# Performance work log

Measured on AMD Instinct MI355X. Metric: run time of the kernel, lower is better.

## Reference

```python
import jax, jax.numpy as jnp
import numpy as np
import math

B, S, HID = 1, 2048, 2048
H, QLR, KVLR = 16, 1536, 512
NOPE, ROPE, VD = 128, 64, 128
QKD = NOPE + ROPE


def rmsnorm(x, w, eps=1e-6):
    v = jnp.mean(x * x, axis=-1, keepdims=True)
    return w * (x * jax.lax.rsqrt(v + eps))


def rope_tables(seq_len, dim):
    inv_freq = 1.0 / (10000.0 ** (jnp.arange(0, dim, 2, dtype=jnp.float32) / dim))
    t = jnp.arange(seq_len, dtype=jnp.float32)[:, None]
    freqs = t * inv_freq[None, :]
    freqs = jnp.concatenate([freqs, freqs], axis=-1)  # [S, dim]
    return jnp.cos(freqs), jnp.sin(freqs)


def rotate_half(x):
    x1, x2 = jnp.split(x, 2, axis=-1)
    return jnp.concatenate([-x2, x1], axis=-1)


def setup_inputs() -> dict:
    key = jax.random.key(0)
    ks = jax.random.split(key, 8)
    s = 0.02
    return {
        'x': jax.random.normal(ks[0], (B, S, HID), jnp.float32),
        'wq_a_w': jax.random.normal(ks[1], (QLR, HID), jnp.float32) * s,
        'wq_a_b': jnp.zeros((QLR,), jnp.float32),
        'q_norm_w': jnp.ones((QLR,), jnp.float32),
        'wq_b_w': jax.random.normal(ks[2], (H * QKD, QLR), jnp.float32) * s,
        'wq_b_b': jnp.zeros((H * QKD,), jnp.float32),
        'wkv_a_w': jax.random.normal(ks[3], (KVLR + ROPE, HID), jnp.float32) * s,
        'wkv_a_b': jnp.zeros((KVLR + ROPE,), jnp.float32),
        'kv_norm_w': jnp.ones((KVLR,), jnp.float32),
        'wkv_b_w': jax.random.normal(ks[4], (H * (NOPE + VD), KVLR), jnp.float32) * s,
        'wo_w': jax.random.normal(ks[5], (HID, H * VD), jnp.float32) * s,
        'wo_b': jnp.zeros((HID,), jnp.float32),
    }


def reference(x, wq_a_w, wq_a_b, q_norm_w, wq_b_w, wq_b_b, wkv_a_w, wkv_a_b,
              kv_norm_w, wkv_b_w, wo_w, wo_b):
    bs, seq_len, _ = x.shape
    # low-rank q projection
    q = x @ wq_a_w.T + wq_a_b            # [B,S,QLR]
    q = rmsnorm(q, q_norm_w)
    q = q @ wq_b_w.T + wq_b_b            # [B,S,H*QKD]
    q = q.reshape(bs, seq_len, H, QKD)
    q_nope, q_pe = q[..., :NOPE], q[..., NOPE:]

    # latent kv + rope key
    kv_full = x @ wkv_a_w.T + wkv_a_b    # [B,S,KVLR+ROPE]
    kv, k_pe = kv_full[..., :KVLR], kv_full[..., KVLR:]

    cos, sin = rope_tables(seq_len, ROPE)        # [S,ROPE]
    cos4 = cos[None, :, None, :]
    sin4 = sin[None, :, None, :]
    q_pe = q_pe * cos4 + rotate_half(q_pe) * sin4          # [B,S,H,ROPE]
    k_pe = k_pe * cos[None] + rotate_half(k_pe) * sin[None]  # [B,S,ROPE]

    # absorbed kv projection
    wkv_b = wkv_b_w.reshape(H, NOPE + VD, KVLR)
    q_nope = jnp.einsum('bshd,hdc->bshc', q_nope, wkv_b[:, :NOPE])  # [B,S,H,KVLR]
    kv = rmsnorm(kv, kv_norm_w)                                     # [B,T,KVLR]

    scores = (jnp.einsum('bshc,btc->bsht', q_nope, kv)
              + jnp.einsum('bshr,btr->bsht', q_pe, k_pe)) / math.sqrt(QKD)
    # causal mask: position t > s masked
    s_idx = jnp.arange(seq_len)
    mask = jnp.where(s_idx[None, :, None, None] >= s_idx[None, None, None, :],
                     0.0, -jnp.inf)  # [1,S,1,T]
    scores = jax.nn.softmax(scores + mask, axis=-1)

    out = jnp.einsum('bsht,btc->bshc', scores, kv)            # [B,S,H,KVLR]
    out = jnp.einsum('bshc,hdc->bshd', out, wkv_b[:, NOPE:])  # [B,S,H,VD]
    out = out.reshape(bs, seq_len, H * VD)
    return out @ wo_w.T + wo_b
```

## Files before the change

kernel.cpp:

```cpp
#include <hip/hip_runtime.h>
#include <hip/hip_bf16.h>
#include <stdint.h>


using bf16 = __hip_bfloat16;
typedef __bf16 bf16x8 __attribute__((ext_vector_type(8)));
typedef __bf16 bf16x4 __attribute__((ext_vector_type(4)));
typedef float f32x4 __attribute__((ext_vector_type(4)));

#define S_LEN 2048
#define NHEAD 16

static __device__ __forceinline__ void gload16(const void* g, void* l) {
  __builtin_amdgcn_global_load_lds(
      (const __attribute__((address_space(1))) unsigned int*)g,
      (__attribute__((address_space(3))) unsigned int*)l, 16, 0, 0);
}

__global__ void cvt_all(const float* __restrict__ x, const float* __restrict__ wqa_s,
                        const float* __restrict__ wqb_s, const float* __restrict__ wkva_s,
                        const float* __restrict__ wkvb_s, const float* __restrict__ wo_s,
                        bf16* __restrict__ xb, bf16* __restrict__ wqa,
                        bf16* __restrict__ wqb, bf16* __restrict__ wkva,
                        bf16* __restrict__ wkvb, bf16* __restrict__ wob) {
  const size_t n0 = 1048576;
  const size_t n1 = n0 + 786432;
  const size_t n2 = n1 + 1179648;
  const size_t n3 = n2 + 327680;
  const size_t n4 = n3 + 524288;
  const size_t n5 = n4 + 1048576;
  auto cvt4 = [](const float4 v, bf16* d) {
    bf16x4 o;
    o[0] = (__bf16)__float2bfloat16(v.x);
    o[1] = (__bf16)__float2bfloat16(v.y);
    o[2] = (__bf16)__float2bfloat16(v.z);
    o[3] = (__bf16)__float2bfloat16(v.w);
    *(bf16x4*)d = o;
  };
  for (size_t i = (size_t)blockIdx.x * blockDim.x + threadIdx.x; i < n5;
       i += (size_t)gridDim.x * blockDim.x) {
    if (i < n0) {
      cvt4(*(const float4*)(x + i * 4), xb + i * 4);
    } else if (i < n1) {
      size_t j = i - n0;
      cvt4(*(const float4*)(wqa_s + j * 4), wqa + j * 4);
    } else if (i < n2) {
      size_t j = i - n1;
      cvt4(*(const float4*)(wqb_s + j * 4), wqb + j * 4);
    } else if (i < n3) {
      size_t j = i - n2;
      size_t e = j * 4;
      int r = (int)(e / 2048), c = (int)(e % 2048);
      float4 v = (r < 576) ? *(const float4*)(wkva_s + (size_t)r * 2048 + c)
                           : make_float4(0.f, 0.f, 0.f, 0.f);
      cvt4(v, wkva + e);
    } else if (i < n4) {
      size_t j = i - n3;
      cvt4(*(const float4*)(wkvb_s + j * 4), wkvb + j * 4);
    } else {
      size_t j = i - n4;
      cvt4(*(const float4*)(wo_s + j * 4), wob + j * 4);
    }
  }
}

__global__ void rmsnorm_bf16(const bf16* __restrict__ in, const float* __restrict__ w,
                             bf16* __restrict__ out, int cols) {
  const int r = blockIdx.x, tid = threadIdx.x;
  const bf16* row = in + (size_t)r * cols;
  float ss = 0.f;
  for (int c = tid; c < cols; c += 256) {
    float v = __bfloat162float(row[c]);
    ss += v * v;
  }
  for (int m = 32; m >= 1; m >>= 1) ss += __shfl_xor(ss, m, 64);
  __shared__ float red[4];
  if ((tid & 63) == 0) red[tid >> 6] = ss;
  __syncthreads();
  ss = red[0] + red[1] + red[2] + red[3];
  float inv = rsqrtf(ss / (float)cols + 1e-6f);
  for (int c = tid; c < cols; c += 256)
    out[(size_t)r * cols + c] = __float2bfloat16(__bfloat162float(row[c]) * inv * w[c]);
}

__global__ void kv_post(const float* __restrict__ kvf, const float* __restrict__ kvw,
                        bf16* __restrict__ kvn, bf16* __restrict__ Kh) {
  const int t = blockIdx.x, tid = threadIdx.x;
  const float* row = kvf + (size_t)t * 640;
  float ss = 0.f;
  for (int c = tid; c < 512; c += 256) { float v = row[c]; ss += v * v; }
  for (int m = 32; m >= 1; m >>= 1) ss += __shfl_xor(ss, m, 64);
  __shared__ float red[4];
  if ((tid & 63) == 0) red[tid >> 6] = ss;
  __syncthreads();
  ss = red[0] + red[1] + red[2] + red[3];
  float inv = rsqrtf(ss * (1.0f / 512.0f) + 1e-6f);
  for (int c = tid; c < 512; c += 256)
    kvn[(size_t)t * 512 + c] = __float2bfloat16(row[c] * inv * kvw[c]);
  if (tid < 32) {
    const int j = tid;
    float freq = expf(-(float)j * (1.0f / 32.0f) * 9.210340371976184f);
    float ang = (float)t * freq;
    float cs = cosf(ang), sn = sinf(ang);
    float x1 = row[512 + j];
    float x2 = row[512 + j + 32];
    bf16 o1 = __float2bfloat16(x1 * cs - x2 * sn);
    bf16 o2 = __float2bfloat16(x2 * cs + x1 * sn);
#pragma unroll
    for (int h = 0; h < 16; ++h) {
      bf16* kr = Kh + ((size_t)h * S_LEN + t) * 192 + 128;
      kr[j] = o1;
      kr[j + 32] = o2;
    }
  }
}

__global__ void q_rope(bf16* __restrict__ qv) {
  const int s = blockIdx.x, tid = threadIdx.x;
  for (int it = tid; it < 512; it += 256) {
    const int h = it >> 5, j = it & 31;
    float freq = expf(-(float)j * (1.0f / 32.0f) * 9.210340371976184f);
    float ang = (float)s * freq;
    float cs = cosf(ang), sn = sinf(ang);
    bf16* base = qv + (size_t)s * 3072 + h * 192 + 128;
    float x1 = __bfloat162float(base[j]);
    float x2 = __bfloat162float(base[j + 32]);
    base[j] = __float2bfloat16(x1 * cs - x2 * sn);
    base[j + 32] = __float2bfloat16(x2 * cs + x1 * sn);
  }
}

__global__ __launch_bounds__(256, 2)
void attn_flash(const bf16* __restrict__ qv, const bf16* __restrict__ Kh,
                const bf16* __restrict__ V2T, bf16* __restrict__ oabs) {
  const int lin = (int)blockIdx.x + 32 * (int)blockIdx.y;
  const int l2 = (lin & 7) * 64 + (lin >> 3);
  const int h = l2 >> 5;
  const int qb = 31 - (l2 & 31);
  const int tid = threadIdx.x, w = tid >> 6, lane = tid & 63;
  const int lo = lane & 15, hi = lane >> 4;
  __shared__ bf16 Kn[2][64 * 128];
  __shared__ bf16 Vt[2][128 * 64];
  __shared__ bf16 Pl[4][16 * 72];
  const int q0 = qb * 64 + w * 16;
  const int q = q0 + lo;

  bf16x8 Qf[6];
  {
    const bf16* qp = qv + (size_t)(q0 + lo) * 3072 + h * 192 + hi * 8;
#pragma unroll
    for (int ks = 0; ks < 6; ++ks) Qf[ks] = *(const bf16x8*)(qp + ks * 32);
  }
  f32x4 o[8];
#pragma unroll
  for (int cg = 0; cg < 8; ++cg) o[cg] = (f32x4){0.f, 0.f, 0.f, 0.f};
  float mrow = -3e38f, lrow = 0.f;

  const bf16* khh = Kh + (size_t)h * S_LEN * 192;
  const bf16* vth = V2T + (size_t)h * 128 * S_LEN;

  auto stage = [&](int tt, int b) {
    const int t0s = tt * 64;
#pragma unroll
    for (int i = 0; i < 4; ++i) {
      const int c = w * 4 + i;
      const int row = c * 4 + (lane >> 4);
      gload16(khh + (size_t)(t0s + row) * 192 + (((lane & 15) ^ (row & 7)) << 3),
              &Kn[b][c * 512]);
    }
#pragma unroll
    for (int i = 0; i < 4; ++i) {
      const int c = w * 4 + i;
      const int row = c * 8 + (lane >> 3);
      gload16(vth + (size_t)row * S_LEN + t0s + (((lane & 7) ^ (row & 7)) << 3),
              &Vt[b][c * 512]);
    }
  };

  const int ntile = qb + 1;
  stage(0, 0);
  for (int t = 0; t < ntile; ++t) {
    __syncthreads();
    const int b = t & 1;
    const int t0 = t * 64;

    bf16x8 rk[2][4];
#pragma unroll
    for (int ks2 = 0; ks2 < 2; ++ks2)
#pragma unroll
      for (int f = 0; f < 4; ++f)
        rk[ks2][f] = *(const bf16x8*)(khh + (size_t)(t0 + f * 16 + lo) * 192 + 128 +
                                      ks2 * 32 + hi * 8);

    if (t + 1 < ntile) stage(t + 1, b ^ 1);

    f32x4 sc[4];
#pragma unroll
    for (int f = 0; f < 4; ++f) sc[f] = (f32x4){0.f, 0.f, 0.f, 0.f};
#pragma unroll
    for (int ks = 0; ks < 4; ++ks)
#pragma unroll
      for (int f = 0; f < 4; ++f) {
        const int row = f * 16 + lo;
        bf16x8 kf = *(const bf16x8*)&Kn[b][row * 128 + ((((ks << 2) + hi) ^ (row & 7)) << 3)];
        sc[f] = __builtin_amdgcn_mfma_f32_16x16x32_bf16(kf, Qf[ks], sc[f], 0, 0, 0);
      }
#pragma unroll
    for (int ks2 = 0; ks2 < 2; ++ks2)
#pragma unroll
      for (int f = 0; f < 4; ++f)
        sc[f] = __builtin_amdgcn_mfma_f32_16x16x32_bf16(rk[ks2][f], Qf[4 + ks2], sc[f], 0, 0, 0);

    const bool diag = (t == qb);
    float rmax = -3e38f;
#pragma unroll
    for (int f = 0; f < 4; ++f)
#pragma unroll
      for (int j = 0; j < 4; ++j) {
        float v = sc[f][j] * 0.0721687836487032f;
        if (diag && (t0 + f * 16 + hi * 4 + j > q)) v = -3e38f;
        sc[f][j] = v;
        rmax = fmaxf(rmax, v);
      }
    rmax = fmaxf(rmax, __shfl_xor(rmax, 16, 64));
    rmax = fmaxf(rmax, __shfl_xor(rmax, 32, 64));

    if (!__all(rmax <= mrow)) {
      const float mn = fmaxf(mrow, rmax);
      const float fsc = __expf(mrow - mn);
      mrow = mn;
      lrow *= fsc;
      float fscO[4];
#pragma unroll
      for (int j = 0; j < 4; ++j) fscO[j] = __shfl(fsc, hi * 4 + j, 64);
#pragma unroll
      for (int cg = 0; cg < 8; ++cg)
#pragma unroll
        for (int j = 0; j < 4; ++j) o[cg][j] *= fscO[j];
    }

    float rsum = 0.f;
    bf16* prow = &Pl[w][lo * 72];
#pragma unroll
    for (int f = 0; f < 4; ++f) {
      float pj[4];
#pragma unroll
      for (int j = 0; j < 4; ++j) {
        pj[j] = __expf(sc[f][j] - mrow);
        rsum += pj[j];
      }
#pragma unroll
      for (int i2 = 0; i2 < 2; ++i2) {
        uint32_t lo16 = (uint32_t)__bfloat16_as_ushort(__float2bfloat16(pj[i2 * 2]));
        uint32_t hi16 = (uint32_t)__bfloat16_as_ushort(__float2bfloat16(pj[i2 * 2 + 1]));
        *(uint32_t*)(prow + f * 16 + hi * 4 + i2 * 2) = lo16 | (hi16 << 16);
      }
    }
    rsum += __shfl_xor(rsum, 16, 64);
    rsum += __shfl_xor(rsum, 32, 64);
    lrow += rsum;

#pragma unroll
    for (int tk = 0; tk < 2; ++tk) {
      bf16x8 pa = *(const bf16x8*)&Pl[w][lo * 72 + tk * 32 + hi * 8];
#pragma unroll
      for (int cg = 0; cg < 8; ++cg) {
        const int vrow = cg * 16 + lo;
        bf16x8 vf = *(const bf16x8*)&Vt[b][vrow * 64 + ((((tk << 2) + hi) ^ (vrow & 7)) << 3)];
        o[cg] = __builtin_amdgcn_mfma_f32_16x16x32_bf16(pa, vf, o[cg], 0, 0, 0);
      }
    }
  }

  const float linv = 1.0f / lrow;
  float linvO[4];
#pragma unroll
  for (int j = 0; j < 4; ++j) linvO[j] = __shfl(linv, hi * 4 + j, 64);
  bf16* ob = oabs + (size_t)q0 * 2048 + h * 128;
#pragma unroll
  for (int j = 0; j < 4; ++j)
#pragma unroll
    for (int cg = 0; cg < 8; ++cg)
      ob[(size_t)(hi * 4 + j) * 2048 + cg * 16 + lo] =
          __float2bfloat16(o[cg][j] * linvO[j]);
}

template <bool BIAS, bool BF16OUT, int BM>
__global__ __launch_bounds__(256)
void gemm_bt(const bf16* __restrict__ A, const bf16* __restrict__ B,
             const float* __restrict__ bias, void* __restrict__ Cv,
             int lda, int ldb, int ldc, int K, int Nreal,
             long long bA, long long bB, long long bC, int mode) {
  int bx, byi, bz;
  {
    const int gx = gridDim.x, gy = gridDim.y;
    const int nwg = gx * gy * (int)gridDim.z;
    const int lin = (int)blockIdx.x + gx * ((int)blockIdx.y + gy * (int)blockIdx.z);
    const int cpx = nwg >> 3;
    const int l2 = (lin & 7) * cpx + (lin >> 3);
    bx = l2 % gx;
    byi = (l2 / gx) % gy;
    bz = l2 / (gx * gy);
    if (mode) byi = (bz & 1) ? byi : gy - 1 - byi;
  }
  const size_t m0 = (size_t)byi * BM, n0 = (size_t)bx * 128;
  if (mode == 1 && (int)n0 >= (int)m0 + BM) return;
  const int Keff = (mode == 2) ? ((K < (int)m0 + BM) ? K : (int)m0 + BM) : K;

  constexpr int ACH = BM / 8;
  constexpr int PER = (ACH + 16) / 4;
  constexpr int NFR = (BM == 64) ? 2 : 4;
  __shared__ bf16 As[2][BM * 64];
  __shared__ bf16 Bs[2][8192];
  const int tid = threadIdx.x;
  const int wave = tid >> 6, lane = tid & 63;
  const int lo = lane & 15, hi = lane >> 4;
  const int rowbase = (BM == 64) ? 0 : ((wave >> 1) * 64);
  const int colbase = (BM == 64) ? (wave * 32) : ((wave & 1) * 64);
  A += (size_t)bz * (size_t)bA;
  B += (size_t)bz * (size_t)bB;
  const int srow = lane >> 3;
  const int scol = (((lane & 7) ^ srow) * 8);
  const int rsw = lo & 7;

  auto stage = [&](int k0, int buf) {
#pragma unroll
    for (int i = 0; i < PER; ++i) {
      const int blk = wave * PER + i;
      if (blk < ACH) {
        const int row = blk * 8 + srow;
        gload16(A + (m0 + row) * (size_t)lda + k0 + scol, &As[buf][blk * 512]);
      } else {
        const int j = blk - ACH;
        const int row = j * 8 + srow;
        gload16(B + (n0 + row) * (size_t)ldb + k0 + scol, &Bs[buf][j * 512]);
      }
    }
  };

  f32x4 acc[4][NFR] = {};
  stage(0, 0);
  int cur = 0;
  for (int k0 = 0; k0 < Keff; k0 += 64) {
    __syncthreads();
    if (k0 + 64 < Keff) stage(k0 + 64, cur ^ 1);
#pragma unroll
    for (int kk = 0; kk < 2; ++kk) {
      const int ch = (((kk << 2) + hi) ^ rsw) << 3;
      bf16x8 af[4], bfr[NFR];
#pragma unroll
      for (int m = 0; m < 4; ++m)
        af[m] = *(const bf16x8*)&As[cur][(rowbase + m * 16 + lo) * 64 + ch];
#pragma unroll
      for (int n = 0; n < NFR; ++n)
        bfr[n] = *(const bf16x8*)&Bs[cur][(colbase + n * 16 + lo) * 64 + ch];
#pragma unroll
      for (int m = 0; m < 4; ++m)
#pragma unroll
        for (int n = 0; n < NFR; ++n)
          acc[m][n] = __builtin_amdgcn_mfma_f32_16x16x32_bf16(af[m], bfr[n], acc[m][n], 0, 0, 0);
    }
    cur ^= 1;
  }
  float* Cf = (float*)Cv;
  bf16* Cb = (bf16*)Cv;
  const size_t cbase = (size_t)bz * (size_t)bC;
#pragma unroll
  for (int m = 0; m < 4; ++m) {
    const size_t row = m0 + rowbase + m * 16 + hi * 4;
#pragma unroll
    for (int n = 0; n < NFR; ++n) {
      const int col = (int)n0 + colbase + n * 16 + lo;
      if (col < Nreal) {
        const float bv = BIAS ? bias[col] : 0.0f;
#pragma unroll
        for (int j = 0; j < 4; ++j) {
          const float v = acc[m][n][j] + bv;
          const size_t off = cbase + (row + j) * (size_t)ldc + col;
          if (BF16OUT) Cb[off] = __float2bfloat16(v);
          else         Cf[off] = v;
        }
      }
    }
  }
}

extern "C" void kernel_launch(void* const* d_in, const int* in_sizes, int n_in,
                              void* d_out, int out_size, void* d_ws, size_t ws_size,
                              hipStream_t stream) {
  const float* x       = (const float*)d_in[0];
  const float* wq_a_w  = (const float*)d_in[1];
  const float* wq_a_b  = (const float*)d_in[2];
  const float* q_norm  = (const float*)d_in[3];
  const float* wq_b_w  = (const float*)d_in[4];
  const float* wq_b_b  = (const float*)d_in[5];
  const float* wkv_a_w = (const float*)d_in[6];
  const float* wkv_a_b = (const float*)d_in[7];
  const float* kv_norm = (const float*)d_in[8];
  const float* wkv_b_w = (const float*)d_in[9];
  const float* wo_w    = (const float*)d_in[10];
  const float* wo_bias = (const float*)d_in[11];
  float* out = (float*)d_out;

  char* base = (char*)d_ws;
  bf16*  xb   = (bf16*)(base + 0);
  bf16*  wqa  = (bf16*)(base + 8388608);
  bf16*  wqb  = (bf16*)(base + 14680064);
  bf16*  wkva = (bf16*)(base + 24117248);
  bf16*  wkvb = (bf16*)(base + 26738688);
  bf16*  qa   = (bf16*)(base + 30932992);
  bf16*  qn   = (bf16*)(base + 37224448);
  float* kvf  = (float*)(base + 43515904);
  bf16*  kvn  = (bf16*)(base + 48758784);
  char* q = base + 134217728;
  bf16* qv   = (bf16*)(q);             q += 12582912;
  bf16* Kh   = (bf16*)(q);             q += 12582912;
  bf16* V2T  = (bf16*)(q);             q += 8388608;
  bf16* wob  = (bf16*)(q);             q += 8388608;
  bf16* oabs = (bf16*)(q);             q += 8388608;

  cvt_all<<<dim3(2048), 256, 0, stream>>>(x, wq_a_w, wq_b_w, wkv_a_w, wkv_b_w, wo_w,
                                          xb, wqa, wqb, wkva, wkvb, wob);

  gemm_bt<true, true, 64><<<dim3(12, 32, 1), 256, 0, stream>>>(
      xb, wqa, wq_a_b, qa, 2048, 2048, 1536, 2048, 1536, 0, 0, 0, 0);
  rmsnorm_bf16<<<2048, 256, 0, stream>>>(qa, q_norm, qn, 1536);
  gemm_bt<true, true, 128><<<dim3(24, 16, 1), 256, 0, stream>>>(
      qn, wqb, wq_b_b, qv, 1536, 1536, 3072, 1536, 3072, 0, 0, 0, 0);
  q_rope<<<2048, 256, 0, stream>>>(qv);
  gemm_bt<true, false, 64><<<dim3(5, 32, 1), 256, 0, stream>>>(
      xb, wkva, wkv_a_b, kvf, 2048, 2048, 640, 2048, 576, 0, 0, 0, 0);
  kv_post<<<2048, 256, 0, stream>>>(kvf, kv_norm, kvn, Kh);
  gemm_bt<false, true, 64><<<dim3(1, 32, 16), 256, 0, stream>>>(
      kvn, wkvb, nullptr, Kh, 512, 512, 192, 512, 128,
      0, 256ll * 512, 2048ll * 192, 0);
  gemm_bt<false, true, 64><<<dim3(16, 2, 16), 256, 0, stream>>>(
      wkvb + 128ull * 512, kvn, nullptr, V2T, 512, 512, 2048, 512, 2048,
      256ll * 512, 0, 128ll * 2048, 0);

  attn_flash<<<dim3(32, 16), 256, 0, stream>>>(qv, Kh, V2T, oabs);

  gemm_bt<true, false, 64><<<dim3(16, 32, 1), 256, 0, stream>>>(
      oabs, wob, wo_bias, out, 2048, 2048, 2048, 2048, 2048, 0, 0, 0, 0);
}
```

Baseline: 251.3 us.

## Split causal attention over KV range into two partitions with separate combine kernel

Replaces the single flash-attention kernel with a split-KV version that launches twice as many workgroups, each handling half of the causal key tiles for a query block and head. It writes unnormalized fp32 partial outputs plus row max and sum. A new combine kernel merges the two halves with log-sum-exp rescaling and writes bf16 output. The goal is more parallelism and better load balance across CUs for the triangular workload, at the cost of extra fp32 traffic, a second launch, and a workspace buffer. It also moves the prefetch stage ahead of the rope-key register loads.

```diff
diff --git a/kernel.cpp b/kernel.cpp
--- a/kernel.cpp
+++ b/kernel.cpp
@@ -131,12 +131,13 @@
 }
 
 __global__ __launch_bounds__(256, 2)
-void attn_flash(const bf16* __restrict__ qv, const bf16* __restrict__ Kh,
-                const bf16* __restrict__ V2T, bf16* __restrict__ oabs) {
-  const int lin = (int)blockIdx.x + 32 * (int)blockIdx.y;
-  const int l2 = (lin & 7) * 64 + (lin >> 3);
-  const int h = l2 >> 5;
-  const int qb = 31 - (l2 & 31);
+void attn_split(const bf16* __restrict__ qv, const bf16* __restrict__ Kh,
+                const bf16* __restrict__ V2T, float* __restrict__ oP,
+                float* __restrict__ mP, float* __restrict__ lP) {
+  const int jb = (int)blockIdx.x;
+  const int h = jb & 15;
+  const int sp = (jb >> 4) & 1;
+  const int qb = 31 - (jb >> 5);
   const int tid = threadIdx.x, w = tid >> 6, lane = tid & 63;
   const int lo = lane & 15, hi = lane >> 4;
   __shared__ bf16 Kn[2][64 * 128];
@@ -177,13 +178,17 @@
     }
   };
 
-  const int ntile = qb + 1;
-  stage(0, 0);
-  for (int t = 0; t < ntile; ++t) {
+  const int nt = qb + 1;
+  const int tb = sp ? (nt >> 1) : 0;
+  const int te = sp ? nt : (nt >> 1);
+  if (tb < te) stage(tb, tb & 1);
+  for (int t = tb; t < te; ++t) {
     __syncthreads();
     const int b = t & 1;
     const int t0 = t * 64;
 
+    if (t + 1 < te) stage(t + 1, b ^ 1);
+
     bf16x8 rk[2][4];
 #pragma unroll
     for (int ks2 = 0; ks2 < 2; ++ks2)
@@ -191,8 +196,6 @@
       for (int f = 0; f < 4; ++f)
         rk[ks2][f] = *(const bf16x8*)(khh + (size_t)(t0 + f * 16 + lo) * 192 + 128 +
                                       ks2 * 32 + hi * 8);
-
-    if (t + 1 < ntile) stage(t + 1, b ^ 1);
 
     f32x4 sc[4];
 #pragma unroll
@@ -272,17 +275,33 @@
     }
   }
 
-  const float linv = 1.0f / lrow;
-  float linvO[4];
-#pragma unroll
-  for (int j = 0; j < 4; ++j) linvO[j] = __shfl(linv, hi * 4 + j, 64);
-  bf16* ob = oabs + (size_t)q0 * 2048 + h * 128;
+  float* op = oP + (((size_t)sp * 16 + h) * S_LEN + q0) * 128;
 #pragma unroll
   for (int j = 0; j < 4; ++j)
 #pragma unroll
     for (int cg = 0; cg < 8; ++cg)
-      ob[(size_t)(hi * 4 + j) * 2048 + cg * 16 + lo] =
-          __float2bfloat16(o[cg][j] * linvO[j]);
+      op[(size_t)(hi * 4 + j) * 128 + cg * 16 + lo] = o[cg][j];
+  if (hi == 0) {
+    const size_t mi = ((size_t)sp * 16 + h) * S_LEN + q0 + lo;
+    mP[mi] = mrow;
+    lP[mi] = lrow;
+  }
+}
+
+__global__ void attn_combine(const float* __restrict__ oP, const float* __restrict__ mP,
+                             const float* __restrict__ lP, bf16* __restrict__ oabs) {
+  const int qq = (int)blockIdx.x * 2 + ((int)threadIdx.x >> 7);
+  const int hh = (int)blockIdx.y;
+  const int d = (int)threadIdx.x & 127;
+  const size_t i0 = (size_t)hh * S_LEN + qq;
+  const size_t i1 = (size_t)(16 + hh) * S_LEN + qq;
+  const float m0 = mP[i0], m1 = mP[i1];
+  const float l0 = lP[i0], l1 = lP[i1];
+  const float M = fmaxf(m0, m1);
+  const float w0 = __expf(m0 - M), w1 = __expf(m1 - M);
+  const float li = 1.0f / (l0 * w0 + l1 * w1);
+  const float v = (oP[i0 * 128 + d] * w0 + oP[i1 * 128 + d] * w1) * li;
+  oabs[(size_t)qq * 2048 + hh * 128 + d] = __float2bfloat16(v);
 }
 
 template <bool BIAS, bool BF16OUT, int BM>
@@ -413,11 +432,14 @@
   float* kvf  = (float*)(base + 43515904);
   bf16*  kvn  = (bf16*)(base + 48758784);
   char* q = base + 134217728;
-  bf16* qv   = (bf16*)(q);             q += 12582912;
-  bf16* Kh   = (bf16*)(q);             q += 12582912;
-  bf16* V2T  = (bf16*)(q);             q += 8388608;
-  bf16* wob  = (bf16*)(q);             q += 8388608;
-  bf16* oabs = (bf16*)(q);             q += 8388608;
+  bf16* qv    = (bf16*)(q);            q += 12582912;
+  bf16* Kh    = (bf16*)(q);            q += 12582912;
+  bf16* V2T   = (bf16*)(q);            q += 8388608;
+  bf16* wob   = (bf16*)(q);            q += 8388608;
+  bf16* oabs  = (bf16*)(q);            q += 8388608;
+  float* oP   = (float*)(q);           q += 33554432;
+  float* mP   = (float*)(q);           q += 262144;
+  float* lP   = (float*)(q);           q += 262144;
 
   cvt_all<<<dim3(2048), 256, 0, stream>>>(x, wq_a_w, wq_b_w, wkv_a_w, wkv_b_w, wo_w,
                                           xb, wqa, wqb, wkva, wkvb, wob);
@@ -438,7 +460,8 @@
       wkvb + 128ull * 512, kvn, nullptr, V2T, 512, 512, 2048, 512, 2048,
       256ll * 512, 0, 128ll * 2048, 0);
 
-  attn_flash<<<dim3(32, 16), 256, 0, stream>>>(qv, Kh, V2T, oabs);
+  attn_split<<<dim3(1024), 256, 0, stream>>>(qv, Kh, V2T, oP, mP, lP);
+  attn_combine<<<dim3(1024, 16), 256, 0, stream>>>(oP, mP, lP, oabs);
 
   gemm_bt<true, false, 64><<<dim3(16, 32, 1), 256, 0, stream>>>(
       oabs, wob, wo_bias, out, 2048, 2048, 2048, 2048, 2048, 0, 0, 0, 0);
```

After: 224.6 us, median of 2. 1.12x faster.
